# Kernel tuning notes

Measured on AMD Instinct MI355X. Metric: run time of the kernel, lower is better.

## Reference

```python
import jax, jax.numpy as jnp
import numpy as np

DIM = 768
HEADS = 12
HIDDEN = 3072
EPS = 1e-5


def _layer_norm(x, g, b):
    mu = jnp.mean(x, axis=-1, keepdims=True)
    var = jnp.mean(jnp.square(x - mu), axis=-1, keepdims=True)
    return (x - mu) * jax.lax.rsqrt(var + EPS) * g + b


def setup_inputs() -> dict:
    key = jax.random.key(0)
    ks = jax.random.split(key, 8)
    s = 0.02
    return {
        "x": jax.random.normal(ks[0], (8, 1024, DIM), dtype=jnp.float32),
        "ln1_g": jnp.ones((DIM,), jnp.float32),
        "ln1_b": jnp.zeros((DIM,), jnp.float32),
        "w_qkv": jax.random.normal(ks[1], (DIM, 3 * DIM), jnp.float32) * s,  # qkv_bias=False
        "w_proj": jax.random.normal(ks[2], (DIM, DIM), jnp.float32) * s,
        "b_proj": jnp.zeros((DIM,), jnp.float32),
        "ln2_g": jnp.ones((DIM,), jnp.float32),
        "ln2_b": jnp.zeros((DIM,), jnp.float32),
        "w_fc1": jax.random.normal(ks[3], (DIM, HIDDEN), jnp.float32) * s,
        "b_fc1": jnp.zeros((HIDDEN,), jnp.float32),
        "w_fc2": jax.random.normal(ks[4], (HIDDEN, DIM), jnp.float32) * s,
        "b_fc2": jnp.zeros((DIM,), jnp.float32),
    }


def reference(x, ln1_g, ln1_b, w_qkv, w_proj, b_proj, ln2_g, ln2_b,
              w_fc1, b_fc1, w_fc2, b_fc2):
    B, S, C = x.shape
    hd = C // HEADS
    scale = hd ** -0.5

    # --- attention branch (pre-norm) ---
    h = _layer_norm(x, ln1_g, ln1_b)
    qkv = (h @ w_qkv).reshape(B, S, 3, HEADS, hd)
    qkv = jnp.transpose(qkv, (2, 0, 3, 1, 4))  # (3, B, H, S, hd)
    q, k, v = qkv[0], qkv[1], qkv[2]
    attn = jnp.einsum("bhqd,bhkd->bhqk", q, k) * scale
    attn = jax.nn.softmax(attn, axis=-1)
    out = jnp.einsum("bhqk,bhkd->bhqd", attn, v)
    out = jnp.transpose(out, (0, 2, 1, 3)).reshape(B, S, C)
    out = out @ w_proj + b_proj
    x = x + out

    # --- MLP branch (pre-norm) ---
    h = _layer_norm(x, ln2_g, ln2_b)
    h = jax.nn.gelu(h @ w_fc1 + b_fc1, approximate=False)
    h = h @ w_fc2 + b_fc2
    return x + h
```

## Files before the change

### kernel.cpp

```cpp
#include <hip/hip_runtime.h>
#include <hip/hip_bf16.h>

#define DIM 768
#define HEADS 12
#define HD 64
#define HIDDEN 3072
#define SEQ 1024
#define NB 8
#define M_TOK (NB * SEQ)
#define C3 (3 * DIM)

typedef __attribute__((ext_vector_type(8))) short short8;
typedef __attribute__((ext_vector_type(4))) short shortx4;
typedef __attribute__((ext_vector_type(4))) float floatx4;

__device__ __forceinline__ void gload_lds16(const void* g, void* l) {
  __builtin_amdgcn_global_load_lds((const __attribute__((address_space(1))) void*)g,
                                   (__attribute__((address_space(3))) void*)l, 16, 0, 0);
}

__device__ __forceinline__ unsigned short bf16b(float f) {
  __hip_bfloat16 h = __float2bfloat16(f);
  return *(unsigned short*)&h;
}

__global__ __launch_bounds__(256) void transpose_cast(
    const float* __restrict__ w, __hip_bfloat16* __restrict__ wt, int K, int N) {
  __shared__ float tile[32][33];
  const int tx = threadIdx.x & 31, ty = threadIdx.x >> 5;
  const int n0 = blockIdx.x * 32, k0 = blockIdx.y * 32;
#pragma unroll
  for (int i = 0; i < 32; i += 8)
    tile[ty + i][tx] = w[(size_t)(k0 + ty + i) * N + n0 + tx];
  __syncthreads();
#pragma unroll
  for (int i = 0; i < 32; i += 8)
    wt[(size_t)(n0 + ty + i) * K + k0 + tx] = __float2bfloat16(tile[tx][ty + i]);
}

__global__ __launch_bounds__(256) void ln_kernel(
    const float* __restrict__ x, const float* __restrict__ gw,
    const float* __restrict__ bw, __hip_bfloat16* __restrict__ outp) {
  const int row = blockIdx.x;
  const int t = threadIdx.x;
  const float* xr = x + (size_t)row * DIM;
  float v0 = xr[t], v1 = xr[t + 256], v2 = xr[t + 512];
  float s = v0 + v1 + v2;
  float sq = v0 * v0 + v1 * v1 + v2 * v2;
#pragma unroll
  for (int m = 1; m < 64; m <<= 1) {
    s += __shfl_xor(s, m);
    sq += __shfl_xor(sq, m);
  }
  __shared__ float ss[4], ssq[4];
  const int wave = t >> 6, lane = t & 63;
  if (lane == 0) { ss[wave] = s; ssq[wave] = sq; }
  __syncthreads();
  s = ss[0] + ss[1] + ss[2] + ss[3];
  sq = ssq[0] + ssq[1] + ssq[2] + ssq[3];
  const float mean = s * (1.f / 768.f);
  const float var = sq * (1.f / 768.f) - mean * mean;
  const float rstd = rsqrtf(var + 1e-5f);
  __hip_bfloat16* orow = outp + (size_t)row * DIM;
  orow[t]       = __float2bfloat16((v0 - mean) * rstd * gw[t]       + bw[t]);
  orow[t + 256] = __float2bfloat16((v1 - mean) * rstd * gw[t + 256] + bw[t + 256]);
  orow[t + 512] = __float2bfloat16((v2 - mean) * rstd * gw[t + 512] + bw[t + 512]);
}

template <int BIAS, int GELU, int RES, int OUTMODE>
__global__ __launch_bounds__(256) void gemm_bt(
    const __hip_bfloat16* __restrict__ A, const __hip_bfloat16* __restrict__ BT,
    const float* __restrict__ bias, const float* __restrict__ resid,
    void* __restrict__ Cout,
    __hip_bfloat16* __restrict__ Qc, __hip_bfloat16* __restrict__ Kc,
    __hip_bfloat16* __restrict__ Vt,
    int M, int N, int K) {
  __shared__ __align__(16) __hip_bfloat16 As[128 * 64];
  __shared__ __align__(16) __hip_bfloat16 Bs[128 * 64];
  const int tid = threadIdx.x;
  const int wave = tid >> 6, lane = tid & 63;
  const int g = lane >> 4, fr = lane & 15;

  const int gx = gridDim.x;
  const int nwg = gx * gridDim.y;
  int bi = blockIdx.y * gx + blockIdx.x;
  bi = (bi & 7) * (nwg >> 3) + (bi >> 3);
  const int m0 = (bi / gx) * 128, n0 = (bi % gx) * 128;
  const int wm = (wave >> 1) * 64, wn = (wave & 1) * 64;

  floatx4 acc[4][4];
  const floatx4 zero = {0.f, 0.f, 0.f, 0.f};
#pragma unroll
  for (int m = 0; m < 4; ++m)
#pragma unroll
    for (int n = 0; n < 4; ++n) acc[m][n] = zero;

  for (int kt = 0; kt < K; kt += 64) {
#pragma unroll
    for (int i = 0; i < 4; ++i) {
      const int li = i * 256 + tid;
      const int row = li >> 3, k8 = (li & 7) << 3;
      gload_lds16(A + (size_t)(m0 + row) * K + kt + k8, As + li * 8);
      gload_lds16(BT + (size_t)(n0 + row) * K + kt + k8, Bs + li * 8);
    }
    __syncthreads();
#pragma unroll
    for (int kk = 0; kk < 64; kk += 32) {
      short8 af[4], bfr[4];
#pragma unroll
      for (int m = 0; m < 4; ++m)
        af[m] = *(const short8*)(As + (wm + m * 16 + fr) * 64 + kk + g * 8);
#pragma unroll
      for (int n = 0; n < 4; ++n)
        bfr[n] = *(const short8*)(Bs + (wn + n * 16 + fr) * 64 + kk + g * 8);
#pragma unroll
      for (int m = 0; m < 4; ++m)
#pragma unroll
        for (int n = 0; n < 4; ++n)
          acc[m][n] = __builtin_amdgcn_mfma_f32_16x16x32_bf16(af[m], bfr[n], acc[m][n], 0, 0, 0);
    }
    __syncthreads();
  }

#pragma unroll
  for (int m = 0; m < 4; ++m) {
    const int row = m0 + wm + m * 16 + g * 4;
#pragma unroll
    for (int n = 0; n < 4; ++n) {
      const int col = n0 + wn + n * 16 + fr;
      if (OUTMODE == 2) {
        const int part = (col >= 1536) ? 2 : (col >= 768 ? 1 : 0);
        const int cc = col - part * 768;
        const int h = cc >> 6, d = cc & 63;
        const int b = row >> 10, s = row & 1023;
        const size_t hb = (size_t)b * HEADS + h;
        if (part == 2) {
          shortx4 pk;
#pragma unroll
          for (int r = 0; r < 4; ++r) pk[r] = (short)bf16b(acc[m][n][r]);
          *(shortx4*)(Vt + (hb * HD + d) * SEQ + s) = pk;
        } else {
          __hip_bfloat16* dst = (part ? Kc : Qc) + (hb * SEQ + s) * HD + d;
#pragma unroll
          for (int r = 0; r < 4; ++r) dst[(size_t)r * HD] = __float2bfloat16(acc[m][n][r]);
        }
      } else {
        const float bv = BIAS ? bias[col] : 0.f;
#pragma unroll
        for (int r = 0; r < 4; ++r) {
          float c = acc[m][n][r] + bv;
          if (GELU) c = 0.5f * c * (1.f + erff(c * 0.70710678118f));
          const size_t off = (size_t)(row + r) * N + col;
          if (RES) c += resid[off];
          if (OUTMODE == 1) ((__hip_bfloat16*)Cout)[off] = __float2bfloat16(c);
          else              ((float*)Cout)[off] = c;
        }
      }
    }
  }
}

__global__ __launch_bounds__(256) void attn_kernel(
    const __hip_bfloat16* __restrict__ Qc, const __hip_bfloat16* __restrict__ Kc,
    const __hip_bfloat16* __restrict__ Vt, __hip_bfloat16* __restrict__ outp) {
  const int tid = threadIdx.x;
  const int wave = tid >> 6, lane = tid & 63;
  const int g = lane >> 4, fr = lane & 15;

  int bi = blockIdx.y * gridDim.x + blockIdx.x;
  bi = (bi & 7) * 192 + (bi >> 3);
  const int qt = bi & 15, bh = bi >> 4;
  const int b = bh / HEADS, h = bh % HEADS;
  const int q0 = qt * 64 + wave * 16;

  const __hip_bfloat16* qp = Qc + ((size_t)bh * SEQ + q0 + fr) * HD;
  const short8 qf0 = *(const short8*)(qp + g * 8);
  const short8 qf1 = *(const short8*)(qp + 32 + g * 8);

  const __hip_bfloat16* kbase = Kc + (size_t)bh * SEQ * HD;
  const __hip_bfloat16* vbase = Vt + (size_t)bh * HD * SEQ;

  __shared__ __align__(16) __hip_bfloat16 Kl[2][64 * 64];
  __shared__ __align__(16) __hip_bfloat16 Vl[2][64 * 64];
  __shared__ __align__(16) char P[4][2048];
  char* const pw = P[wave];
  const int swz = (fr & 7) << 4;
  const int rs3 = fr & 7;

  auto stage = [&](int buf, int kt) {
#pragma unroll
    for (int s = 0; s < 2; ++s) {
      const int idx = s * 256 + tid;
      const int row = idx >> 3, c = idx & 7;
      const int sc = c ^ (row & 7);
      gload_lds16(kbase + (size_t)(kt + row) * HD + sc * 8, &Kl[buf][idx * 8]);
      gload_lds16(vbase + (size_t)row * SEQ + kt + sc * 8, &Vl[buf][idx * 8]);
    }
  };

  float m_r = -1e30f, l_r = 0.f;
  floatx4 acc[4];
  const floatx4 zero = {0.f, 0.f, 0.f, 0.f};
#pragma unroll
  for (int n = 0; n < 4; ++n) acc[n] = zero;

  stage(0, 0);
  asm volatile("s_waitcnt vmcnt(0)" ::: "memory");
  __builtin_amdgcn_s_barrier();

  int cur = 0;
  for (int kt = 0; kt < SEQ; kt += 64) {
    if (kt + 64 < SEQ) stage(cur ^ 1, kt + 64);
    const __hip_bfloat16* kl = Kl[cur];
    const __hip_bfloat16* vl = Vl[cur];

    floatx4 sa[4];
#pragma unroll
    for (int t = 0; t < 4; ++t) {
      const int row = t * 16 + fr;
      const short8 k0 = *(const short8*)(kl + row * 64 + ((g ^ rs3) << 3));
      const short8 k1 = *(const short8*)(kl + row * 64 + (((4 + g) ^ rs3) << 3));
      sa[t] = __builtin_amdgcn_mfma_f32_16x16x32_bf16(k0, qf0, zero, 0, 0, 0);
      sa[t] = __builtin_amdgcn_mfma_f32_16x16x32_bf16(k1, qf1, sa[t], 0, 0, 0);
    }
    float mx = -1e30f;
#pragma unroll
    for (int t = 0; t < 4; ++t)
#pragma unroll
      for (int r = 0; r < 4; ++r) mx = fmaxf(mx, sa[t][r]);
    mx *= 0.125f;
    mx = fmaxf(mx, __shfl_xor(mx, 16));
    mx = fmaxf(mx, __shfl_xor(mx, 32));
    const float mn = fmaxf(m_r, mx);
    const float alpha = __expf(m_r - mn);
    float rsum = 0.f;
#pragma unroll
    for (int t = 0; t < 4; ++t)
#pragma unroll
      for (int r2 = 0; r2 < 4; r2 += 2) {
        const float p0 = __expf(sa[t][r2]     * 0.125f - mn);
        const float p1 = __expf(sa[t][r2 + 1] * 0.125f - mn);
        rsum += p0 + p1;
        const unsigned int word = ((unsigned int)bf16b(p1) << 16) | bf16b(p0);
        const int k = t * 16 + g * 4 + r2;
        *(unsigned int*)(pw + fr * 128 + ((k * 2) ^ swz)) = word;
      }
    rsum += __shfl_xor(rsum, 16);
    rsum += __shfl_xor(rsum, 32);
    l_r = l_r * alpha + rsum;
    m_r = mn;
#pragma unroll
    for (int n = 0; n < 4; ++n) acc[n] *= alpha;
    asm volatile("s_waitcnt lgkmcnt(0)" ::: "memory");
    __builtin_amdgcn_sched_barrier(0);
    const short8 pb0 = *(const short8*)(pw + fr * 128 + ((g * 16)      ^ swz));
    const short8 pb1 = *(const short8*)(pw + fr * 128 + ((64 + g * 16) ^ swz));
#pragma unroll
    for (int n = 0; n < 4; ++n) {
      const int d = n * 16 + fr;
      const short8 va0 = *(const short8*)(vl + d * 64 + ((g ^ rs3) << 3));
      const short8 va1 = *(const short8*)(vl + d * 64 + (((4 + g) ^ rs3) << 3));
      acc[n] = __builtin_amdgcn_mfma_f32_16x16x32_bf16(va0, pb0, acc[n], 0, 0, 0);
      acc[n] = __builtin_amdgcn_mfma_f32_16x16x32_bf16(va1, pb1, acc[n], 0, 0, 0);
    }
    asm volatile("s_waitcnt vmcnt(0) lgkmcnt(0)" ::: "memory");
    __builtin_amdgcn_s_barrier();
    cur ^= 1;
  }

  const float inv_l = 1.f / l_r;
  __hip_bfloat16* op = outp + (size_t)(b * SEQ + q0 + fr) * DIM + h * HD + g * 4;
#pragma unroll
  for (int n = 0; n < 4; ++n) {
    shortx4 pk;
#pragma unroll
    for (int r = 0; r < 4; ++r) pk[r] = (short)bf16b(acc[n][r] * inv_l);
    *(shortx4*)(op + n * 16) = pk;
  }
}

extern "C" void kernel_launch(void* const* d_in, const int* in_sizes, int n_in,
                              void* d_out, int out_size, void* d_ws, size_t ws_size,
                              hipStream_t stream) {
  (void)in_sizes; (void)n_in; (void)out_size; (void)ws_size;
  const float* x      = (const float*)d_in[0];
  const float* ln1_g  = (const float*)d_in[1];
  const float* ln1_b  = (const float*)d_in[2];
  const float* w_qkv  = (const float*)d_in[3];
  const float* w_proj = (const float*)d_in[4];
  const float* b_proj = (const float*)d_in[5];
  const float* ln2_g  = (const float*)d_in[6];
  const float* ln2_b  = (const float*)d_in[7];
  const float* w_fc1  = (const float*)d_in[8];
  const float* b_fc1  = (const float*)d_in[9];
  const float* w_fc2  = (const float*)d_in[10];
  const float* b_fc2  = (const float*)d_in[11];
  float* outp = (float*)d_out;

  char* ws = (char*)d_ws;
  size_t off = 0;
  auto alloc = [&](size_t bytes) -> void* {
    void* p = ws + off;
    off += (bytes + 255) & ~(size_t)255;
    return p;
  };
  __hip_bfloat16* h1     = (__hip_bfloat16*)alloc((size_t)M_TOK * DIM * 2);
  __hip_bfloat16* Qc     = (__hip_bfloat16*)alloc((size_t)M_TOK * DIM * 2);
  __hip_bfloat16* Kc     = (__hip_bfloat16*)alloc((size_t)M_TOK * DIM * 2);
  __hip_bfloat16* Vt     = (__hip_bfloat16*)alloc((size_t)M_TOK * DIM * 2);
  __hip_bfloat16* att    = (__hip_bfloat16*)alloc((size_t)M_TOK * DIM * 2);
  __hip_bfloat16* h2     = (__hip_bfloat16*)alloc((size_t)M_TOK * DIM * 2);
  __hip_bfloat16* act    = (__hip_bfloat16*)alloc((size_t)M_TOK * HIDDEN * 2);
  __hip_bfloat16* wqkvT  = (__hip_bfloat16*)alloc((size_t)C3 * DIM * 2);
  __hip_bfloat16* wprojT = (__hip_bfloat16*)alloc((size_t)DIM * DIM * 2);
  __hip_bfloat16* wfc1T  = (__hip_bfloat16*)alloc((size_t)HIDDEN * DIM * 2);
  __hip_bfloat16* wfc2T  = (__hip_bfloat16*)alloc((size_t)DIM * HIDDEN * 2);
  float* x_mid = outp;

  transpose_cast<<<dim3(C3 / 32, DIM / 32), 256, 0, stream>>>(w_qkv, wqkvT, DIM, C3);
  transpose_cast<<<dim3(DIM / 32, DIM / 32), 256, 0, stream>>>(w_proj, wprojT, DIM, DIM);
  transpose_cast<<<dim3(HIDDEN / 32, DIM / 32), 256, 0, stream>>>(w_fc1, wfc1T, DIM, HIDDEN);
  transpose_cast<<<dim3(DIM / 32, HIDDEN / 32), 256, 0, stream>>>(w_fc2, wfc2T, HIDDEN, DIM);

  ln_kernel<<<M_TOK, 256, 0, stream>>>(x, ln1_g, ln1_b, h1);
  gemm_bt<0, 0, 0, 2><<<dim3(C3 / 128, M_TOK / 128), 256, 0, stream>>>(
      h1, wqkvT, nullptr, nullptr, nullptr, Qc, Kc, Vt, M_TOK, C3, DIM);
  attn_kernel<<<dim3(SEQ / 64, NB * HEADS), 256, 0, stream>>>(Qc, Kc, Vt, att);
  gemm_bt<1, 0, 1, 0><<<dim3(DIM / 128, M_TOK / 128), 256, 0, stream>>>(
      att, wprojT, b_proj, x, x_mid, nullptr, nullptr, nullptr, M_TOK, DIM, DIM);
  ln_kernel<<<M_TOK, 256, 0, stream>>>(x_mid, ln2_g, ln2_b, h2);
  gemm_bt<1, 1, 0, 1><<<dim3(HIDDEN / 128, M_TOK / 128), 256, 0, stream>>>(
      h2, wfc1T, b_fc1, nullptr, act, nullptr, nullptr, nullptr, M_TOK, HIDDEN, DIM);
  gemm_bt<1, 0, 1, 0><<<dim3(DIM / 128, M_TOK / 128), 256, 0, stream>>>(
      act, wfc2T, b_fc2, x_mid, outp, nullptr, nullptr, nullptr, M_TOK, DIM, HIDDEN);
}
```

Baseline: 430.2 us.

## Add double-buffered 256x256 GEMM with swizzled LDS and split-K atomics for FC2

Adds a new 512-thread GEMM kernel with 256x256 output tiles and two LDS buffers. The next K-slab is loaded while the current one is multiplied, and the LDS layout is XOR-swizzled to avoid bank conflicts. The kernel also raises wave priority around the MFMA bursts. It replaces the QKV, FC1 and FC2 GEMMs. FC2 is split four ways along K and accumulates into the output, which already holds the residual, using float atomicAdd. This is meant to raise data reuse and overlap memory with math, at the cost of 128KB of LDS per block (one block per CU), a nondeterministic summation order, and atomic traffic.

```diff
diff --git a/kernel.cpp b/kernel.cpp
--- a/kernel.cpp
+++ b/kernel.cpp
@@ -67,67 +67,110 @@
   orow[t + 512] = __float2bfloat16((v2 - mean) * rstd * gw[t + 512] + bw[t + 512]);
 }
 
-template <int BIAS, int GELU, int RES, int OUTMODE>
-__global__ __launch_bounds__(256) void gemm_bt(
+template <int BIAS, int GELU, int OUTMODE>
+__global__ __launch_bounds__(512, 2) void gemm256(
     const __hip_bfloat16* __restrict__ A, const __hip_bfloat16* __restrict__ BT,
-    const float* __restrict__ bias, const float* __restrict__ resid,
-    void* __restrict__ Cout,
+    const float* __restrict__ bias, void* __restrict__ Cout,
     __hip_bfloat16* __restrict__ Qc, __hip_bfloat16* __restrict__ Kc,
     __hip_bfloat16* __restrict__ Vt,
-    int M, int N, int K) {
-  __shared__ __align__(16) __hip_bfloat16 As[128 * 64];
-  __shared__ __align__(16) __hip_bfloat16 Bs[128 * 64];
+    int N, int K) {
+  __shared__ __align__(16) __hip_bfloat16 Al[2][256 * 64];
+  __shared__ __align__(16) __hip_bfloat16 Bl[2][256 * 64];
   const int tid = threadIdx.x;
   const int wave = tid >> 6, lane = tid & 63;
   const int g = lane >> 4, fr = lane & 15;
+  const int wm = wave >> 2, wn = wave & 3;
 
   const int gx = gridDim.x;
   const int nwg = gx * gridDim.y;
   int bi = blockIdx.y * gx + blockIdx.x;
   bi = (bi & 7) * (nwg >> 3) + (bi >> 3);
-  const int m0 = (bi / gx) * 128, n0 = (bi % gx) * 128;
-  const int wm = (wave >> 1) * 64, wn = (wave & 1) * 64;
-
-  floatx4 acc[4][4];
+  const int m0 = (bi / gx) * 256, n0 = (bi % gx) * 256;
+  const int k0 = blockIdx.z * 768;
+
+  auto stage = [&](int slot, int kt) {
+#pragma unroll
+    for (int i = 0; i < 4; ++i) {
+      const int idx = i * 512 + tid;
+      const int row = idx >> 3, c = idx & 7;
+      const int sc = (c ^ (row & 7)) << 3;
+      gload_lds16(A + (size_t)(m0 + row) * K + kt + sc, &Al[slot][idx * 8]);
+    }
+#pragma unroll
+    for (int i = 0; i < 4; ++i) {
+      const int idx = i * 512 + tid;
+      const int row = idx >> 3, c = idx & 7;
+      const int sc = (c ^ (row & 7)) << 3;
+      gload_lds16(BT + (size_t)(n0 + row) * K + kt + sc, &Bl[slot][idx * 8]);
+    }
+  };
+
+  floatx4 acc[8][4];
   const floatx4 zero = {0.f, 0.f, 0.f, 0.f};
 #pragma unroll
-  for (int m = 0; m < 4; ++m)
-#pragma unroll
-    for (int n = 0; n < 4; ++n) acc[m][n] = zero;
-
-  for (int kt = 0; kt < K; kt += 64) {
-#pragma unroll
-    for (int i = 0; i < 4; ++i) {
-      const int li = i * 256 + tid;
-      const int row = li >> 3, k8 = (li & 7) << 3;
-      gload_lds16(A + (size_t)(m0 + row) * K + kt + k8, As + li * 8);
-      gload_lds16(BT + (size_t)(n0 + row) * K + kt + k8, Bs + li * 8);
-    }
-    __syncthreads();
-#pragma unroll
-    for (int kk = 0; kk < 64; kk += 32) {
-      short8 af[4], bfr[4];
-#pragma unroll
-      for (int m = 0; m < 4; ++m)
-        af[m] = *(const short8*)(As + (wm + m * 16 + fr) * 64 + kk + g * 8);
-#pragma unroll
-      for (int n = 0; n < 4; ++n)
-        bfr[n] = *(const short8*)(Bs + (wn + n * 16 + fr) * 64 + kk + g * 8);
-#pragma unroll
-      for (int m = 0; m < 4; ++m)
-#pragma unroll
-        for (int n = 0; n < 4; ++n)
-          acc[m][n] = __builtin_amdgcn_mfma_f32_16x16x32_bf16(af[m], bfr[n], acc[m][n], 0, 0, 0);
-    }
-    __syncthreads();
-  }
-
-#pragma unroll
-  for (int m = 0; m < 4; ++m) {
-    const int row = m0 + wm + m * 16 + g * 4;
-#pragma unroll
-    for (int n = 0; n < 4; ++n) {
-      const int col = n0 + wn + n * 16 + fr;
+  for (int mf = 0; mf < 8; ++mf)
+#pragma unroll
+    for (int nf = 0; nf < 4; ++nf) acc[mf][nf] = zero;
+
+  stage(0, k0);
+  stage(1, k0 + 64);
+  asm volatile("s_waitcnt vmcnt(8)" ::: "memory");
+  __builtin_amdgcn_s_barrier();
+  asm volatile("" ::: "memory");
+
+#pragma unroll 1
+  for (int t = 0; t < 12; ++t) {
+    const __hip_bfloat16* Ab = Al[t & 1];
+    const __hip_bfloat16* Bb = Bl[t & 1];
+    short8 bfr[4][2];
+#pragma unroll
+    for (int nf = 0; nf < 4; ++nf)
+#pragma unroll
+      for (int kh = 0; kh < 2; ++kh) {
+        const int row = wn * 64 + nf * 16 + fr;
+        bfr[nf][kh] = *(const short8*)(Bb + row * 64 + (((kh * 4 + g) ^ (row & 7)) << 3));
+      }
+#pragma unroll
+    for (int p = 0; p < 4; ++p) {
+      short8 afr[2][2];
+#pragma unroll
+      for (int s = 0; s < 2; ++s)
+#pragma unroll
+        for (int kh = 0; kh < 2; ++kh) {
+          const int row = wm * 128 + (p * 2 + s) * 16 + fr;
+          afr[s][kh] = *(const short8*)(Ab + row * 64 + (((kh * 4 + g) ^ (row & 7)) << 3));
+        }
+      __builtin_amdgcn_s_setprio(1);
+#pragma unroll
+      for (int s = 0; s < 2; ++s)
+#pragma unroll
+        for (int nf = 0; nf < 4; ++nf)
+#pragma unroll
+          for (int kh = 0; kh < 2; ++kh)
+            acc[p * 2 + s][nf] = __builtin_amdgcn_mfma_f32_16x16x32_bf16(
+                afr[s][kh], bfr[nf][kh], acc[p * 2 + s][nf], 0, 0, 0);
+      __builtin_amdgcn_s_setprio(0);
+    }
+    if (t == 11) break;
+    asm volatile("" ::: "memory");
+    __builtin_amdgcn_s_barrier();
+    asm volatile("" ::: "memory");
+    if (t + 2 < 12) {
+      stage(t & 1, k0 + (t + 2) * 64);
+      asm volatile("s_waitcnt vmcnt(8)" ::: "memory");
+    } else {
+      asm volatile("s_waitcnt vmcnt(0)" ::: "memory");
+    }
+    __builtin_amdgcn_s_barrier();
+    asm volatile("" ::: "memory");
+  }
+
+#pragma unroll
+  for (int mf = 0; mf < 8; ++mf) {
+    const int row = m0 + wm * 128 + mf * 16 + g * 4;
+#pragma unroll
+    for (int nf = 0; nf < 4; ++nf) {
+      const int col = n0 + wn * 64 + nf * 16 + fr;
       if (OUTMODE == 2) {
         const int part = (col >= 1536) ? 2 : (col >= 768 ? 1 : 0);
         const int cc = col - part * 768;
@@ -137,24 +180,99 @@
         if (part == 2) {
           shortx4 pk;
 #pragma unroll
-          for (int r = 0; r < 4; ++r) pk[r] = (short)bf16b(acc[m][n][r]);
+          for (int r = 0; r < 4; ++r) pk[r] = (short)bf16b(acc[mf][nf][r]);
           *(shortx4*)(Vt + (hb * HD + d) * SEQ + s) = pk;
         } else {
           __hip_bfloat16* dst = (part ? Kc : Qc) + (hb * SEQ + s) * HD + d;
 #pragma unroll
-          for (int r = 0; r < 4; ++r) dst[(size_t)r * HD] = __float2bfloat16(acc[m][n][r]);
+          for (int r = 0; r < 4; ++r) dst[(size_t)r * HD] = __float2bfloat16(acc[mf][nf][r]);
         }
+      } else if (OUTMODE == 3) {
+        const float bv = (BIAS && blockIdx.z == 0) ? bias[col] : 0.f;
+#pragma unroll
+        for (int r = 0; r < 4; ++r)
+          atomicAdd((float*)Cout + (size_t)(row + r) * N + col, acc[mf][nf][r] + bv);
       } else {
         const float bv = BIAS ? bias[col] : 0.f;
 #pragma unroll
         for (int r = 0; r < 4; ++r) {
-          float c = acc[m][n][r] + bv;
+          float c = acc[mf][nf][r] + bv;
           if (GELU) c = 0.5f * c * (1.f + erff(c * 0.70710678118f));
-          const size_t off = (size_t)(row + r) * N + col;
-          if (RES) c += resid[off];
-          if (OUTMODE == 1) ((__hip_bfloat16*)Cout)[off] = __float2bfloat16(c);
-          else              ((float*)Cout)[off] = c;
+          ((__hip_bfloat16*)Cout)[(size_t)(row + r) * N + col] = __float2bfloat16(c);
         }
+      }
+    }
+  }
+}
+
+template <int BIAS, int GELU, int RES, int OUTMODE>
+__global__ __launch_bounds__(256) void gemm_bt(
+    const __hip_bfloat16* __restrict__ A, const __hip_bfloat16* __restrict__ BT,
+    const float* __restrict__ bias, const float* __restrict__ resid,
+    void* __restrict__ Cout,
+    int M, int N, int K) {
+  __shared__ __align__(16) __hip_bfloat16 As[128 * 64];
+  __shared__ __align__(16) __hip_bfloat16 Bs[128 * 64];
+  const int tid = threadIdx.x;
+  const int wave = tid >> 6, lane = tid & 63;
+  const int g = lane >> 4, fr = lane & 15;
+
+  const int gx = gridDim.x;
+  const int nwg = gx * gridDim.y;
+  int bi = blockIdx.y * gx + blockIdx.x;
+  bi = (bi & 7) * (nwg >> 3) + (bi >> 3);
+  const int m0 = (bi / gx) * 128, n0 = (bi % gx) * 128;
+  const int wm = (wave >> 1) * 64, wn = (wave & 1) * 64;
+
+  floatx4 acc[4][4];
+  const floatx4 zero = {0.f, 0.f, 0.f, 0.f};
+#pragma unroll
+  for (int m = 0; m < 4; ++m)
+#pragma unroll
+    for (int n = 0; n < 4; ++n) acc[m][n] = zero;
+
+  for (int kt = 0; kt < K; kt += 64) {
+#pragma unroll
+    for (int i = 0; i < 4; ++i) {
+      const int li = i * 256 + tid;
+      const int row = li >> 3, k8 = (li & 7) << 3;
+      gload_lds16(A + (size_t)(m0 + row) * K + kt + k8, As + li * 8);
+      gload_lds16(BT + (size_t)(n0 + row) * K + kt + k8, Bs + li * 8);
+    }
+    __syncthreads();
+#pragma unroll
+    for (int kk = 0; kk < 64; kk += 32) {
+      short8 af[4], bfr[4];
+#pragma unroll
+      for (int m = 0; m < 4; ++m)
+        af[m] = *(const short8*)(As + (wm + m * 16 + fr) * 64 + kk + g * 8);
+#pragma unroll
+      for (int n = 0; n < 4; ++n)
+        bfr[n] = *(const short8*)(Bs + (wn + n * 16 + fr) * 64 + kk + g * 8);
+#pragma unroll
+      for (int m = 0; m < 4; ++m)
+#pragma unroll
+        for (int n = 0; n < 4; ++n)
+          acc[m][n] = __builtin_amdgcn_mfma_f32_16x16x32_bf16(af[m], bfr[n], acc[m][n], 0, 0, 0);
+    }
+    __syncthreads();
+  }
+
+#pragma unroll
+  for (int m = 0; m < 4; ++m) {
+    const int row = m0 + wm + m * 16 + g * 4;
+#pragma unroll
+    for (int n = 0; n < 4; ++n) {
+      const int col = n0 + wn + n * 16 + fr;
+      const float bv = BIAS ? bias[col] : 0.f;
+#pragma unroll
+      for (int r = 0; r < 4; ++r) {
+        float c = acc[m][n][r] + bv;
+        if (GELU) c = 0.5f * c * (1.f + erff(c * 0.70710678118f));
+        const size_t off = (size_t)(row + r) * N + col;
+        if (RES) c += resid[off];
+        if (OUTMODE == 1) ((__hip_bfloat16*)Cout)[off] = __float2bfloat16(c);
+        else              ((float*)Cout)[off] = c;
       }
     }
   }
@@ -323,14 +441,14 @@
   transpose_cast<<<dim3(DIM / 32, HIDDEN / 32), 256, 0, stream>>>(w_fc2, wfc2T, HIDDEN, DIM);
 
   ln_kernel<<<M_TOK, 256, 0, stream>>>(x, ln1_g, ln1_b, h1);
-  gemm_bt<0, 0, 0, 2><<<dim3(C3 / 128, M_TOK / 128), 256, 0, stream>>>(
-      h1, wqkvT, nullptr, nullptr, nullptr, Qc, Kc, Vt, M_TOK, C3, DIM);
+  gemm256<0, 0, 2><<<dim3(C3 / 256, M_TOK / 256), 512, 0, stream>>>(
+      h1, wqkvT, nullptr, nullptr, Qc, Kc, Vt, C3, DIM);
   attn_kernel<<<dim3(SEQ / 64, NB * HEADS), 256, 0, stream>>>(Qc, Kc, Vt, att);
   gemm_bt<1, 0, 1, 0><<<dim3(DIM / 128, M_TOK / 128), 256, 0, stream>>>(
-      att, wprojT, b_proj, x, x_mid, nullptr, nullptr, nullptr, M_TOK, DIM, DIM);
+      att, wprojT, b_proj, x, x_mid, M_TOK, DIM, DIM);
   ln_kernel<<<M_TOK, 256, 0, stream>>>(x_mid, ln2_g, ln2_b, h2);
-  gemm_bt<1, 1, 0, 1><<<dim3(HIDDEN / 128, M_TOK / 128), 256, 0, stream>>>(
-      h2, wfc1T, b_fc1, nullptr, act, nullptr, nullptr, nullptr, M_TOK, HIDDEN, DIM);
-  gemm_bt<1, 0, 1, 0><<<dim3(DIM / 128, M_TOK / 128), 256, 0, stream>>>(
-      act, wfc2T, b_fc2, x_mid, outp, nullptr, nullptr, nullptr, M_TOK, DIM, HIDDEN);
-}
+  gemm256<1, 1, 1><<<dim3(HIDDEN / 256, M_TOK / 256), 512, 0, stream>>>(
+      h2, wfc1T, b_fc1, act, nullptr, nullptr, nullptr, HIDDEN, DIM);
+  gemm256<1, 0, 3><<<dim3(DIM / 256, M_TOK / 256, 4), 512, 0, stream>>>(
+      act, wfc2T, b_fc2, outp, nullptr, nullptr, nullptr, DIM, HIDDEN);
+}
```

After: 472.6 us. 1.1x slower.

## Replace GEMM with 4-slot LDS ring pipeline, swizzled layout, larger tiles

Applied to the files above, without the earlier changes.

Replaces the synchronous load-then-compute GEMM with a templated kernel. It keeps a 4-slot LDS ring of K=32 tiles, issued three stages ahead with direct global-to-LDS loads, and uses explicit vmcnt waits and one barrier per step. LDS rows are XOR-swizzled to reduce bank conflicts, and MFMA sections are raised in priority with s_setprio. The QKV and FC1 GEMMs move to 256x256 tiles with 512 threads, which take 128KB of LDS per block and so may limit occupancy to one block per CU. The wait counts are tuned by hand to the per-thread load count.

```diff
diff --git a/kernel.cpp b/kernel.cpp
--- a/kernel.cpp
+++ b/kernel.cpp
@@ -67,67 +67,102 @@
   orow[t + 512] = __float2bfloat16((v2 - mean) * rstd * gw[t + 512] + bw[t + 512]);
 }
 
-template <int BIAS, int GELU, int RES, int OUTMODE>
-__global__ __launch_bounds__(256) void gemm_bt(
+template <int BM, int BN, int WM, int WN, int OUTMODE, int BIAS, int GELU>
+__global__ __launch_bounds__(WM * WN * 64, 2) void gemm_ring(
     const __hip_bfloat16* __restrict__ A, const __hip_bfloat16* __restrict__ BT,
     const float* __restrict__ bias, const float* __restrict__ resid,
     void* __restrict__ Cout,
     __hip_bfloat16* __restrict__ Qc, __hip_bfloat16* __restrict__ Kc,
     __hip_bfloat16* __restrict__ Vt,
-    int M, int N, int K) {
-  __shared__ __align__(16) __hip_bfloat16 As[128 * 64];
-  __shared__ __align__(16) __hip_bfloat16 Bs[128 * 64];
+    int N, int K) {
+  constexpr int THREADS = WM * WN * 64;
+  constexpr int MF = BM / WM / 16, NF = BN / WN / 16;
+  constexpr int SLOT = (BM + BN) * 32;
+  __shared__ __align__(16) __hip_bfloat16 ring[4 * SLOT];
+
   const int tid = threadIdx.x;
   const int wave = tid >> 6, lane = tid & 63;
   const int g = lane >> 4, fr = lane & 15;
+  const int wm = wave / WN, wn = wave % WN;
 
   const int gx = gridDim.x;
   const int nwg = gx * gridDim.y;
   int bi = blockIdx.y * gx + blockIdx.x;
   bi = (bi & 7) * (nwg >> 3) + (bi >> 3);
-  const int m0 = (bi / gx) * 128, n0 = (bi % gx) * 128;
-  const int wm = (wave >> 1) * 64, wn = (wave & 1) * 64;
-
-  floatx4 acc[4][4];
+  const int m0 = (bi / gx) * BM, n0 = (bi % gx) * BN;
+
+  auto stage = [&](int slot, int kt) {
+    __hip_bfloat16* dst = ring + slot * SLOT;
+#pragma unroll
+    for (int i = 0; i < BM * 4 / THREADS; ++i) {
+      const int idx = i * THREADS + tid;
+      const int row = idx >> 2, pc = idx & 3;
+      const int lc = pc ^ ((row >> 1) & 3);
+      gload_lds16(A + (size_t)(m0 + row) * K + kt + lc * 8, dst + idx * 8);
+    }
+    __hip_bfloat16* dstB = dst + BM * 32;
+#pragma unroll
+    for (int i = 0; i < BN * 4 / THREADS; ++i) {
+      const int idx = i * THREADS + tid;
+      const int row = idx >> 2, pc = idx & 3;
+      const int lc = pc ^ ((row >> 1) & 3);
+      gload_lds16(BT + (size_t)(n0 + row) * K + kt + lc * 8, dstB + idx * 8);
+    }
+  };
+
+  floatx4 acc[MF][NF];
   const floatx4 zero = {0.f, 0.f, 0.f, 0.f};
 #pragma unroll
-  for (int m = 0; m < 4; ++m)
-#pragma unroll
-    for (int n = 0; n < 4; ++n) acc[m][n] = zero;
-
-  for (int kt = 0; kt < K; kt += 64) {
-#pragma unroll
-    for (int i = 0; i < 4; ++i) {
-      const int li = i * 256 + tid;
-      const int row = li >> 3, k8 = (li & 7) << 3;
-      gload_lds16(A + (size_t)(m0 + row) * K + kt + k8, As + li * 8);
-      gload_lds16(BT + (size_t)(n0 + row) * K + kt + k8, Bs + li * 8);
-    }
-    __syncthreads();
-#pragma unroll
-    for (int kk = 0; kk < 64; kk += 32) {
-      short8 af[4], bfr[4];
-#pragma unroll
-      for (int m = 0; m < 4; ++m)
-        af[m] = *(const short8*)(As + (wm + m * 16 + fr) * 64 + kk + g * 8);
-#pragma unroll
-      for (int n = 0; n < 4; ++n)
-        bfr[n] = *(const short8*)(Bs + (wn + n * 16 + fr) * 64 + kk + g * 8);
-#pragma unroll
-      for (int m = 0; m < 4; ++m)
-#pragma unroll
-        for (int n = 0; n < 4; ++n)
-          acc[m][n] = __builtin_amdgcn_mfma_f32_16x16x32_bf16(af[m], bfr[n], acc[m][n], 0, 0, 0);
-    }
-    __syncthreads();
-  }
-
-#pragma unroll
-  for (int m = 0; m < 4; ++m) {
-    const int row = m0 + wm + m * 16 + g * 4;
-#pragma unroll
-    for (int n = 0; n < 4; ++n) {
-      const int col = n0 + wn + n * 16 + fr;
+  for (int mf = 0; mf < MF; ++mf)
+#pragma unroll
+    for (int nf = 0; nf < NF; ++nf) acc[mf][nf] = zero;
+
+  const int NT = K >> 5;
+  stage(0, 0);
+  stage(1, 32);
+  stage(2, 64);
+
+#pragma unroll 1
+  for (int t = 0; t < NT; ++t) {
+    asm volatile("s_waitcnt lgkmcnt(0)" ::: "memory");
+    if (t < NT - 2)       asm volatile("s_waitcnt vmcnt(8)" ::: "memory");
+    else if (t == NT - 2) asm volatile("s_waitcnt vmcnt(4)" ::: "memory");
+    else                  asm volatile("s_waitcnt vmcnt(0)" ::: "memory");
+    __builtin_amdgcn_s_barrier();
+    if (t + 3 < NT) stage((t + 3) & 3, (t + 3) * 32);
+
+    const __hip_bfloat16* Ab = ring + (t & 3) * SLOT;
+    const __hip_bfloat16* Bb = Ab + BM * 32;
+    short8 bfr[NF];
+#pragma unroll
+    for (int nf = 0; nf < NF; ++nf) {
+      const int row = wn * (BN / WN) + nf * 16 + fr;
+      const int pc = g ^ ((row >> 1) & 3);
+      bfr[nf] = *(const short8*)(Bb + row * 32 + pc * 8);
+    }
+    short8 afr[MF];
+#pragma unroll
+    for (int mf = 0; mf < MF; ++mf) {
+      const int row = wm * (BM / WM) + mf * 16 + fr;
+      const int pc = g ^ ((row >> 1) & 3);
+      afr[mf] = *(const short8*)(Ab + row * 32 + pc * 8);
+    }
+    __builtin_amdgcn_s_setprio(1);
+#pragma unroll
+    for (int mf = 0; mf < MF; ++mf)
+#pragma unroll
+      for (int nf = 0; nf < NF; ++nf)
+        acc[mf][nf] = __builtin_amdgcn_mfma_f32_16x16x32_bf16(
+            afr[mf], bfr[nf], acc[mf][nf], 0, 0, 0);
+    __builtin_amdgcn_s_setprio(0);
+  }
+
+#pragma unroll
+  for (int mf = 0; mf < MF; ++mf) {
+    const int row = m0 + wm * (BM / WM) + mf * 16 + g * 4;
+#pragma unroll
+    for (int nf = 0; nf < NF; ++nf) {
+      const int col = n0 + wn * (BN / WN) + nf * 16 + fr;
       if (OUTMODE == 2) {
         const int part = (col >= 1536) ? 2 : (col >= 768 ? 1 : 0);
         const int cc = col - part * 768;
@@ -137,23 +172,25 @@
         if (part == 2) {
           shortx4 pk;
 #pragma unroll
-          for (int r = 0; r < 4; ++r) pk[r] = (short)bf16b(acc[m][n][r]);
+          for (int r = 0; r < 4; ++r) pk[r] = (short)bf16b(acc[mf][nf][r]);
           *(shortx4*)(Vt + (hb * HD + d) * SEQ + s) = pk;
         } else {
           __hip_bfloat16* dst = (part ? Kc : Qc) + (hb * SEQ + s) * HD + d;
 #pragma unroll
-          for (int r = 0; r < 4; ++r) dst[(size_t)r * HD] = __float2bfloat16(acc[m][n][r]);
+          for (int r = 0; r < 4; ++r) dst[(size_t)r * HD] = __float2bfloat16(acc[mf][nf][r]);
         }
       } else {
         const float bv = BIAS ? bias[col] : 0.f;
 #pragma unroll
         for (int r = 0; r < 4; ++r) {
-          float c = acc[m][n][r] + bv;
+          float c = acc[mf][nf][r] + bv;
           if (GELU) c = 0.5f * c * (1.f + erff(c * 0.70710678118f));
           const size_t off = (size_t)(row + r) * N + col;
-          if (RES) c += resid[off];
-          if (OUTMODE == 1) ((__hip_bfloat16*)Cout)[off] = __float2bfloat16(c);
-          else              ((float*)Cout)[off] = c;
+          if (OUTMODE == 1) {
+            ((__hip_bfloat16*)Cout)[off] = __float2bfloat16(c);
+          } else {
+            ((float*)Cout)[off] = c + resid[off];
+          }
         }
       }
     }
@@ -323,14 +360,14 @@
   transpose_cast<<<dim3(DIM / 32, HIDDEN / 32), 256, 0, stream>>>(w_fc2, wfc2T, HIDDEN, DIM);
 
   ln_kernel<<<M_TOK, 256, 0, stream>>>(x, ln1_g, ln1_b, h1);
-  gemm_bt<0, 0, 0, 2><<<dim3(C3 / 128, M_TOK / 128), 256, 0, stream>>>(
-      h1, wqkvT, nullptr, nullptr, nullptr, Qc, Kc, Vt, M_TOK, C3, DIM);
+  gemm_ring<256, 256, 2, 4, 2, 0, 0><<<dim3(C3 / 256, M_TOK / 256), 512, 0, stream>>>(
+      h1, wqkvT, nullptr, nullptr, nullptr, Qc, Kc, Vt, C3, DIM);
   attn_kernel<<<dim3(SEQ / 64, NB * HEADS), 256, 0, stream>>>(Qc, Kc, Vt, att);
-  gemm_bt<1, 0, 1, 0><<<dim3(DIM / 128, M_TOK / 128), 256, 0, stream>>>(
-      att, wprojT, b_proj, x, x_mid, nullptr, nullptr, nullptr, M_TOK, DIM, DIM);
+  gemm_ring<128, 128, 2, 2, 0, 1, 0><<<dim3(DIM / 128, M_TOK / 128), 256, 0, stream>>>(
+      att, wprojT, b_proj, x, x_mid, nullptr, nullptr, nullptr, DIM, DIM);
   ln_kernel<<<M_TOK, 256, 0, stream>>>(x_mid, ln2_g, ln2_b, h2);
-  gemm_bt<1, 1, 0, 1><<<dim3(HIDDEN / 128, M_TOK / 128), 256, 0, stream>>>(
-      h2, wfc1T, b_fc1, nullptr, act, nullptr, nullptr, nullptr, M_TOK, HIDDEN, DIM);
-  gemm_bt<1, 0, 1, 0><<<dim3(DIM / 128, M_TOK / 128), 256, 0, stream>>>(
-      act, wfc2T, b_fc2, x_mid, outp, nullptr, nullptr, nullptr, M_TOK, DIM, HIDDEN);
-}
+  gemm_ring<256, 256, 2, 4, 1, 1, 1><<<dim3(HIDDEN / 256, M_TOK / 256), 512, 0, stream>>>(
+      h2, wfc1T, b_fc1, nullptr, act, nullptr, nullptr, nullptr, HIDDEN, DIM);
+  gemm_ring<128, 128, 2, 2, 0, 1, 0><<<dim3(DIM / 128, M_TOK / 128), 256, 0, stream>>>(
+      act, wfc2T, b_fc2, x_mid, outp, nullptr, nullptr, nullptr, DIM, HIDDEN);
+}
```

Measured after the change: 404.3 us. -6.0%, faster.
